# Performance work log

Measured on AMD Instinct MI355X. Metric: run time of the kernel, lower is better.

Reference implementation:

```python
import jax, jax.numpy as jnp
import numpy as np

DIM = 512
WIN = 8
HEADS = 16
HEAD_DIM = DIM // HEADS
N = WIN * WIN
B_ = 1568


def _rel_pos_idx(window_size: int) -> np.ndarray:
    ch = np.arange(window_size)
    cw = np.arange(window_size)
    coords = np.stack(np.meshgrid(ch, cw, indexing='ij'))  # [2, W, W]
    flat = coords.reshape(2, -1)                            # [2, N]
    rel = flat[:, :, None] - flat[:, None, :]               # [2, N, N]
    rel = rel.transpose(1, 2, 0).copy()                     # [N, N, 2]
    rel[:, :, 0] += window_size - 1
    rel[:, :, 1] += window_size - 1
    rel[:, :, 0] *= 2 * window_size - 1
    return rel.sum(-1).astype(np.int32)                     # [N, N]


def setup_inputs() -> dict:
    key = jax.random.key(0)
    kx, kt, kq, kp, kb = jax.random.split(key, 5)
    x = jax.random.normal(kx, (B_, N, DIM), dtype=jnp.float32)
    # learned params
    table = jax.random.normal(kt, ((2 * WIN - 1) ** 2, HEADS), dtype=jnp.float32) * 0.02
    qkv_w = jax.random.normal(kq, (3 * DIM, DIM), dtype=jnp.float32) * (1.0 / np.sqrt(DIM))
    proj_w = jax.random.normal(kp, (DIM, DIM), dtype=jnp.float32) * (1.0 / np.sqrt(DIM))
    proj_b = jax.random.normal(kb, (DIM,), dtype=jnp.float32) * 0.02
    rel_idx = jnp.asarray(_rel_pos_idx(WIN))  # [N, N] int32
    return {"x": x, "qkv_w": qkv_w, "table": table, "proj_w": proj_w,
            "proj_b": proj_b, "rel_idx": rel_idx}


def reference(x, qkv_w, table, proj_w, proj_b, rel_idx):
    Bw, n, c = x.shape
    scale = jnp.sqrt(jnp.float32(HEAD_DIM))
    # qkv: Linear no-bias, torch weight [3C, C] -> x @ W^T
    qkv = (x @ qkv_w.T).reshape(Bw, n, 3, HEADS, HEAD_DIM)
    qkv = jnp.transpose(qkv, (2, 0, 3, 1, 4))  # [3, B, H, N, hd]
    q, k, v = qkv[0], qkv[1], qkv[2]
    attn = jnp.einsum('bhnd,bhmd->bhnm', q, k) / scale  # [B, H, N, N]
    bias = table[rel_idx]                                # [N, N, H]
    attn = attn + jnp.transpose(bias, (2, 0, 1))[None]   # [B, H, N, N]
    attn = jax.nn.softmax(attn, axis=-1)
    out = jnp.einsum('bhnm,bhmd->bhnd', attn, v)         # [B, H, N, hd]
    out = jnp.transpose(out, (0, 2, 1, 3)).reshape(Bw, n, c)
    return out @ proj_w.T + proj_b
```

## Files before the change

kernel.cpp:

```cpp
#include <hip/hip_runtime.h>
#include <stdint.h>

typedef unsigned short ushort_t;
typedef unsigned long long u64_t;
typedef __attribute__((ext_vector_type(4))) float f32x4;
typedef __attribute__((ext_vector_type(8))) short s16x8;

#define S1_ELEMS ((size_t)1568*64*512)

__device__ __forceinline__ ushort_t f2bf(float f) {
  unsigned u = __builtin_bit_cast(unsigned, f);
  u = u + 0x7fffu + ((u >> 16) & 1u);
  return (ushort_t)(u >> 16);
}

__device__ __forceinline__ void gl_lds16(const ushort_t* g, ushort_t* l) {
  typedef __attribute__((address_space(1))) void gvoid;
  typedef __attribute__((address_space(3))) void lvoid;
  __builtin_amdgcn_global_load_lds((gvoid*)(ushort_t*)g, (lvoid*)l, 16, 0, 0);
}

__global__ void k_prep(const float* __restrict__ x, ushort_t* __restrict__ xh,
                       const float* __restrict__ wq, ushort_t* __restrict__ wqh,
                       const float* __restrict__ wp, ushort_t* __restrict__ wph,
                       const float* __restrict__ table, const int* __restrict__ rel_idx,
                       float* __restrict__ bias) {
  int blk = blockIdx.x, tid = threadIdx.x;
  if (blk < 3136) {
    long i0 = (long)blk*256 + tid;
    #pragma unroll
    for (int rep = 0; rep < 8; rep++) {
      long i = i0 + (long)rep*802816;
      float4 v0 = ((const float4*)x)[2*i];
      float4 v1 = ((const float4*)x)[2*i + 1];
      s16x8 pk;
      pk[0] = (short)f2bf(v0.x); pk[1] = (short)f2bf(v0.y);
      pk[2] = (short)f2bf(v0.z); pk[3] = (short)f2bf(v0.w);
      pk[4] = (short)f2bf(v1.x); pk[5] = (short)f2bf(v1.y);
      pk[6] = (short)f2bf(v1.z); pk[7] = (short)f2bf(v1.w);
      *(s16x8*)&xh[i*8] = pk;
    }
  } else if (blk < 3648) {
    const float* src; ushort_t* dst; long i;
    if (blk < 3520) { src = wq; dst = wqh; i = (long)(blk - 3136)*256 + tid; }
    else            { src = wp; dst = wph; i = (long)(blk - 3520)*256 + tid; }
    float4 v0 = ((const float4*)src)[2*i];
    float4 v1 = ((const float4*)src)[2*i + 1];
    s16x8 pk;
    pk[0] = (short)f2bf(v0.x); pk[1] = (short)f2bf(v0.y);
    pk[2] = (short)f2bf(v0.z); pk[3] = (short)f2bf(v0.w);
    pk[4] = (short)f2bf(v1.x); pk[5] = (short)f2bf(v1.y);
    pk[6] = (short)f2bf(v1.z); pk[7] = (short)f2bf(v1.w);
    *(s16x8*)&dst[i*8] = pk;
  } else {
    int i0 = ((blk - 3648)*256 + tid)*4;
    #pragma unroll
    for (int j = 0; j < 4; j++) {
      int i = i0 + j;
      int h = i >> 12, rc = i & 4095;
      bias[i] = table[rel_idx[rc] * 16 + h];
    }
  }
}

struct GemmCtx {
  ushort_t* lds;
  const ushort_t *pA0, *pA1, *pB0, *pB1;
  int w, lane, wm, wn;
};

template<int BUFP, int KH, int RH, int SSEL, int SBUFP, int SU, int VM, bool BAR>
__device__ __forceinline__ void phase(const GemmCtx& C, f32x4 (&acc)[8][4], s16x8 (&bf)[4], int stau) {
  s16x8 af[4];
  #pragma unroll
  for (int t = 0; t < 4; t++)
    af[t] = *(const s16x8*)&C.lds[BUFP*32768 + ((C.wm*8 + RH*4 + t)*2 + KH)*512 + C.lane*8];
  if constexpr (RH == 0) {
    #pragma unroll
    for (int t = 0; t < 4; t++)
      bf[t] = *(const s16x8*)&C.lds[BUFP*32768 + 16384 + ((C.wn*4 + t)*2 + KH)*512 + C.lane*8];
  }
  if constexpr (SSEL == 0) {
    gl_lds16(C.pA0 + stau*64 + SU*32, C.lds + SBUFP*32768 + (4*C.w + SU)*512);
    gl_lds16(C.pA1 + stau*64 + SU*32, C.lds + SBUFP*32768 + (4*C.w + 2 + SU)*512);
  } else if constexpr (SSEL == 1) {
    gl_lds16(C.pB0 + stau*64 + SU*32, C.lds + SBUFP*32768 + 16384 + (4*C.w + SU)*512);
    gl_lds16(C.pB1 + stau*64 + SU*32, C.lds + SBUFP*32768 + 16384 + (4*C.w + 2 + SU)*512);
  }
  if constexpr (VM == 8) asm volatile("s_waitcnt vmcnt(8)" ::: "memory");
  else if constexpr (VM == 4) asm volatile("s_waitcnt vmcnt(4)" ::: "memory");
  else if constexpr (VM == 0) asm volatile("s_waitcnt vmcnt(0)" ::: "memory");
  __builtin_amdgcn_s_setprio(1);
  #pragma unroll
  for (int ta = 0; ta < 4; ta++)
    #pragma unroll
    for (int tb = 0; tb < 4; tb++)
      acc[RH*4 + ta][tb] = __builtin_amdgcn_mfma_f32_16x16x32_bf16(af[ta], bf[tb], acc[RH*4 + ta][tb], 0, 0, 0);
  __builtin_amdgcn_s_setprio(0);
  if constexpr (BAR) __builtin_amdgcn_s_barrier();
}

template<int BUFP, bool S12, bool S34, int VM2, int VM4>
__device__ __forceinline__ void ktile(const GemmCtx& C, f32x4 (&acc)[8][4], int tau) {
  s16x8 bf[4];
  phase<BUFP, 0, 0, S12 ? 0 : -1, BUFP^1, 1, -1,  false>(C, acc, bf, tau + 1);
  phase<BUFP, 0, 1, S12 ? 1 : -1, BUFP^1, 1, VM2, true >(C, acc, bf, tau + 1);
  phase<BUFP, 1, 0, S34 ? 0 : -1, BUFP,   0, -1,  false>(C, acc, bf, tau + 2);
  phase<BUFP, 1, 1, S34 ? 1 : -1, BUFP,   0, VM4, true >(C, acc, bf, tau + 2);
}

__global__ __launch_bounds__(512, 2) void k_gemm_qkv(
    const ushort_t* __restrict__ xh, const ushort_t* __restrict__ wh,
    ushort_t* __restrict__ qh, ushort_t* __restrict__ kh, ushort_t* __restrict__ vt) {
  extern __shared__ __align__(16) ushort_t lds[];
  const int tid = threadIdx.x, w = tid >> 6, lane = tid & 63;
  const int g = lane >> 4, l15 = lane & 15;
  const int wm = w >> 2, wn = w & 3;
  int flat = blockIdx.x;
  int swz = (flat & 7) * 294 + (flat >> 3);
  int bx = swz % 6, by = swz / 6;

  GemmCtx C;
  C.lds = lds;
  C.pA0 = xh + ((size_t)by*256 + (size_t)(2*w)*16 + l15)*512 + g*8;
  C.pA1 = C.pA0 + 16*512;
  C.pB0 = wh + ((size_t)bx*256 + (size_t)(2*w)*16 + l15)*512 + g*8;
  C.pB1 = C.pB0 + 16*512;
  C.w = w; C.lane = lane; C.wm = wm; C.wn = wn;

  f32x4 acc[8][4];
  #pragma unroll
  for (int r = 0; r < 8; r++)
    #pragma unroll
    for (int c = 0; c < 4; c++) acc[r][c] = (f32x4){0.f, 0.f, 0.f, 0.f};

  gl_lds16(C.pA0 +  0, lds + (4*w + 0)*512);
  gl_lds16(C.pA1 +  0, lds + (4*w + 2)*512);
  gl_lds16(C.pB0 +  0, lds + 16384 + (4*w + 0)*512);
  gl_lds16(C.pB1 +  0, lds + 16384 + (4*w + 2)*512);
  gl_lds16(C.pA0 + 32, lds + (4*w + 1)*512);
  gl_lds16(C.pA1 + 32, lds + (4*w + 3)*512);
  gl_lds16(C.pB0 + 32, lds + 16384 + (4*w + 1)*512);
  gl_lds16(C.pB1 + 32, lds + 16384 + (4*w + 3)*512);
  gl_lds16(C.pA0 + 64, lds + 32768 + (4*w + 0)*512);
  gl_lds16(C.pA1 + 64, lds + 32768 + (4*w + 2)*512);
  gl_lds16(C.pB0 + 64, lds + 32768 + 16384 + (4*w + 0)*512);
  gl_lds16(C.pB1 + 64, lds + 32768 + 16384 + (4*w + 2)*512);
  asm volatile("s_waitcnt vmcnt(4)" ::: "memory");
  __builtin_amdgcn_s_barrier();

  for (int kt = 0; kt < 6; kt += 2) {
    ktile<0, true, true, 8, 8>(C, acc, kt);
    ktile<1, true, true, 8, 8>(C, acc, kt + 1);
  }
  ktile<0, true,  false, 8, 4>(C, acc, 6);
  ktile<1, false, false, 0, -1>(C, acc, 7);

  asm volatile("" ::: "memory");
  const int sel = bx >> 1;
  if (sel < 2) {
    #pragma unroll
    for (int ra = 0; ra < 8; ra++)
      #pragma unroll
      for (int tb = 0; tb < 4; tb++)
        #pragma unroll
        for (int j = 0; j < 4; j++) {
          int row = wm*128 + ra*16 + g*4 + j;
          int col = wn*64 + tb*16 + l15;
          int r = (row >> 6)*8 + (col >> 5);
          int n = row & 63, d = col & 31;
          int byte = r*4096 + ((n*64 + d*2) ^ ((n & 12) << 3));
          *(ushort_t*)((char*)lds + byte) = f2bf(acc[ra][tb][j]);
        }
  } else {
    #pragma unroll
    for (int ra = 0; ra < 8; ra++)
      #pragma unroll
      for (int tb = 0; tb < 4; tb++) {
        int row0 = wm*128 + ra*16 + g*4;
        int col = wn*64 + tb*16 + l15;
        int r = (row0 >> 6)*8 + (col >> 5);
        int n0 = row0 & 63, d = col & 31;
        u64_t pk = (u64_t)f2bf(acc[ra][tb][0])
                 | ((u64_t)f2bf(acc[ra][tb][1]) << 16)
                 | ((u64_t)f2bf(acc[ra][tb][2]) << 32)
                 | ((u64_t)f2bf(acc[ra][tb][3]) << 48);
        int byte = r*4096 + ((d*128 + n0*2) ^ ((d & 7) << 4) ^ (((((d >> 3) ^ (n0 >> 3))) & 1) << 6));
        *(u64_t*)((char*)lds + byte) = pk;
      }
  }
  asm volatile("s_waitcnt lgkmcnt(0)" ::: "memory");
  __builtin_amdgcn_s_barrier();
  ushort_t* dst = (sel == 0) ? qh : (sel == 1) ? kh : vt;
  const int hbase = (bx & 1) * 8;
  #pragma unroll
  for (int it = 0; it < 16; it++) {
    int cg = it*512 + tid;
    int r = cg >> 8, inner = cg & 255;
    int byte;
    if (sel < 2) byte = r*4096 + ((inner*16) ^ (((inner >> 2) & 12) << 3));
    else         byte = r*4096 + ((inner*16) ^ (((inner >> 3) & 7) << 4) ^ ((((inner >> 6) ^ inner) & 1) << 6));
    s16x8 v = *(const s16x8*)((const char*)lds + byte);
    int b = by*4 + (r >> 3), h = hbase + (r & 7);
    *(s16x8*)&dst[(size_t)(b*16 + h)*2048 + inner*8] = v;
  }
}

__device__ __forceinline__ void gemm256_loop(
    ushort_t* lds, const ushort_t* pA, const ushort_t* pB,
    int w, int lane, int wm, int wn, f32x4 (&acc)[8][4]) {
  #pragma unroll
  for (int q = 0; q < 2; q++) {
    gl_lds16(pA + q*8192 +  0, lds + ((2*w + q)*2 + 0)*512);
    gl_lds16(pA + q*8192 + 32, lds + ((2*w + q)*2 + 1)*512);
    gl_lds16(pB + q*8192 +  0, lds + 16384 + ((2*w + q)*2 + 0)*512);
    gl_lds16(pB + q*8192 + 32, lds + 16384 + ((2*w + q)*2 + 1)*512);
  }
  asm volatile("s_waitcnt vmcnt(0)" ::: "memory");
  __builtin_amdgcn_s_barrier();

  for (int tau = 0; tau < 8; ++tau) {
    ushort_t* bufR = lds + (tau & 1)*32768;
    ushort_t* bufW = lds + ((tau & 1) ^ 1)*32768;
    if (tau < 7) {
      int ko = (tau + 1)*64;
      #pragma unroll
      for (int q = 0; q < 2; q++) {
        gl_lds16(pA + q*8192 + ko,      bufW + ((2*w + q)*2 + 0)*512);
        gl_lds16(pA + q*8192 + ko + 32, bufW + ((2*w + q)*2 + 1)*512);
        gl_lds16(pB + q*8192 + ko,      bufW + 16384 + ((2*w + q)*2 + 0)*512);
        gl_lds16(pB + q*8192 + ko + 32, bufW + 16384 + ((2*w + q)*2 + 1)*512);
      }
    }
    s16x8 af[4][2], bf[4][2];
    #pragma unroll
    for (int t = 0; t < 4; t++)
      #pragma unroll
      for (int kh = 0; kh < 2; kh++) {
        af[t][kh] = *(const s16x8*)&bufR[((wm*8 + t)*2 + kh)*512 + lane*8];
        bf[t][kh] = *(const s16x8*)&bufR[16384 + ((wn*4 + t)*2 + kh)*512 + lane*8];
      }
    __builtin_amdgcn_s_setprio(1);
    #pragma unroll
    for (int t = 0; t < 4; t++)
      #pragma unroll
      for (int tb = 0; tb < 4; tb++) {
        acc[t][tb] = __builtin_amdgcn_mfma_f32_16x16x32_bf16(af[t][0], bf[tb][0], acc[t][tb], 0, 0, 0);
        acc[t][tb] = __builtin_amdgcn_mfma_f32_16x16x32_bf16(af[t][1], bf[tb][1], acc[t][tb], 0, 0, 0);
      }
    __builtin_amdgcn_s_setprio(0);
    s16x8 ag[4][2];
    #pragma unroll
    for (int t = 0; t < 4; t++)
      #pragma unroll
      for (int kh = 0; kh < 2; kh++)
        ag[t][kh] = *(const s16x8*)&bufR[((wm*8 + 4 + t)*2 + kh)*512 + lane*8];
    __builtin_amdgcn_s_setprio(1);
    #pragma unroll
    for (int t = 0; t < 4; t++)
      #pragma unroll
      for (int tb = 0; tb < 4; tb++) {
        acc[4 + t][tb] = __builtin_amdgcn_mfma_f32_16x16x32_bf16(ag[t][0], bf[tb][0], acc[4 + t][tb], 0, 0, 0);
        acc[4 + t][tb] = __builtin_amdgcn_mfma_f32_16x16x32_bf16(ag[t][1], bf[tb][1], acc[4 + t][tb], 0, 0, 0);
      }
    __builtin_amdgcn_s_setprio(0);
    asm volatile("s_waitcnt vmcnt(0)" ::: "memory");
    __builtin_amdgcn_s_barrier();
  }
}

__global__ __launch_bounds__(512, 2) void k_gemm_proj(
    const ushort_t* __restrict__ ah, const ushort_t* __restrict__ wh,
    const float* __restrict__ pb, float* __restrict__ out) {
  extern __shared__ __align__(16) ushort_t lds[];
  const int tid = threadIdx.x, w = tid >> 6, lane = tid & 63;
  const int g = lane >> 4, l15 = lane & 15;
  const int wm = w >> 2, wn = w & 3;
  int flat = blockIdx.x;
  int swz = (flat & 7) * 98 + (flat >> 3);
  int bx = swz & 1, by = swz >> 1;

  const ushort_t* pA = ah + ((size_t)by*256 + (size_t)(2*w)*16 + l15)*512 + g*8;
  const ushort_t* pB = wh + ((size_t)bx*256 + (size_t)(2*w)*16 + l15)*512 + g*8;

  f32x4 acc[8][4];
  #pragma unroll
  for (int r = 0; r < 8; r++)
    #pragma unroll
    for (int c = 0; c < 4; c++) acc[r][c] = (f32x4){0.f, 0.f, 0.f, 0.f};

  gemm256_loop(lds, pA, pB, w, lane, wm, wn, acc);

  asm volatile("" ::: "memory");
  #pragma unroll
  for (int p = 0; p < 2; p++) {
    if (p) { asm volatile("" ::: "memory"); __builtin_amdgcn_s_barrier(); }
    if (wm == p) {
      #pragma unroll
      for (int ra = 0; ra < 8; ra++)
        #pragma unroll
        for (int tb = 0; tb < 4; tb++)
          #pragma unroll
          for (int j = 0; j < 4; j++) {
            int row = ra*16 + g*4 + j;
            int col = wn*64 + tb*16 + l15;
            int byte = (row*1024 + col*4) ^ ((row & 12) << 2) ^ ((row & 8) << 3);
            *(float*)((char*)lds + byte) = acc[ra][tb][j];
          }
    }
    asm volatile("s_waitcnt lgkmcnt(0)" ::: "memory");
    __builtin_amdgcn_s_barrier();
    #pragma unroll
    for (int it = 0; it < 16; it++) {
      int cg = it*512 + tid;
      int row = cg >> 6, c16 = cg & 63;
      int byte = row*1024 + ((c16*16) ^ ((row & 12) << 2) ^ ((row & 8) << 3));
      f32x4 v = *(const f32x4*)((const char*)lds + byte);
      int ncol = bx*256 + c16*4;
      f32x4 pbv = *(const f32x4*)&pb[ncol];
      v = v + pbv;
      *(f32x4*)&out[(size_t)(by*256 + p*128 + row)*512 + ncol] = v;
    }
  }
}

__global__ __launch_bounds__(256) void k_attn(
    const ushort_t* __restrict__ qh, const ushort_t* __restrict__ kh,
    const ushort_t* __restrict__ vt, const float* __restrict__ bias,
    ushort_t* __restrict__ aoh) {
  __shared__ ushort_t plds[4][64*72];
  __shared__ float blds[64*68];
  const int tid = threadIdx.x, w = tid >> 6, lane = tid & 63;
  const int g = lane >> 4, l15 = lane & 15;
  const int h = blockIdx.x & 15;
  const int b = (blockIdx.x >> 4)*4 + w;
  const size_t base = (size_t)(b*16 + h) * 2048;

  s16x8 qf[4], kf[4];
  #pragma unroll
  for (int t = 0; t < 4; t++) {
    size_t o = base + (size_t)(t*16 + l15)*32 + g*8;
    qf[t] = *(const s16x8*)&qh[o];
    kf[t] = *(const s16x8*)&kh[o];
  }
  s16x8 vf[2][2];
  #pragma unroll
  for (int kt = 0; kt < 2; kt++)
    #pragma unroll
    for (int nt = 0; nt < 2; nt++)
      vf[kt][nt] = *(const s16x8*)&vt[base + (size_t)(nt*16 + l15)*64 + kt*32 + g*8];

  const float* bh_ = bias + ((size_t)h << 12);
  #pragma unroll
  for (int it = 0; it < 4; it++) {
    int idx = it*1024 + tid*4;
    int rr = idx >> 6, cc = idx & 63;
    *(f32x4*)&blds[rr*68 + cc] = *(const f32x4*)&bh_[idx];
  }
  __syncthreads();

  f32x4 s[4][4];
  #pragma unroll
  for (int r = 0; r < 4; r++)
    #pragma unroll
    for (int c = 0; c < 4; c++) s[r][c] = (f32x4){0.f,0.f,0.f,0.f};
  #pragma unroll
  for (int r = 0; r < 4; r++)
    #pragma unroll
    for (int c = 0; c < 4; c++)
      s[r][c] = __builtin_amdgcn_mfma_f32_16x16x32_bf16(qf[r], kf[c], s[r][c], 0, 0, 0);

  const float invs = 0.17677669529663687f;
  #pragma unroll
  for (int r = 0; r < 4; r++)
    #pragma unroll
    for (int c = 0; c < 4; c++)
      #pragma unroll
      for (int j = 0; j < 4; j++) {
        int rr = r*16 + g*4 + j, cc = c*16 + l15;
        s[r][c][j] = s[r][c][j]*invs + blds[rr*68 + cc];
      }

  #pragma unroll
  for (int r = 0; r < 4; r++)
    #pragma unroll
    for (int j = 0; j < 4; j++) {
      float mx = fmaxf(fmaxf(s[r][0][j], s[r][1][j]), fmaxf(s[r][2][j], s[r][3][j]));
      mx = fmaxf(mx, __shfl_xor(mx, 1));
      mx = fmaxf(mx, __shfl_xor(mx, 2));
      mx = fmaxf(mx, __shfl_xor(mx, 4));
      mx = fmaxf(mx, __shfl_xor(mx, 8));
      float p0 = __expf(s[r][0][j]-mx), p1 = __expf(s[r][1][j]-mx);
      float p2 = __expf(s[r][2][j]-mx), p3 = __expf(s[r][3][j]-mx);
      float sum = p0 + p1 + p2 + p3;
      sum += __shfl_xor(sum, 1);
      sum += __shfl_xor(sum, 2);
      sum += __shfl_xor(sum, 4);
      sum += __shfl_xor(sum, 8);
      float rv = 1.0f / sum;
      s[r][0][j] = p0*rv; s[r][1][j] = p1*rv; s[r][2][j] = p2*rv; s[r][3][j] = p3*rv;
    }

  ushort_t* Pm = plds[w];
  #pragma unroll
  for (int r = 0; r < 4; r++)
    #pragma unroll
    for (int c = 0; c < 4; c++)
      #pragma unroll
      for (int j = 0; j < 4; j++) {
        int rr = r*16 + g*4 + j, cc = c*16 + l15;
        Pm[rr*72 + cc] = f2bf(s[r][c][j]);
      }
  s16x8 pf[4][2];
  #pragma unroll
  for (int ta = 0; ta < 4; ta++)
    #pragma unroll
    for (int kt = 0; kt < 2; kt++)
      pf[ta][kt] = *(const s16x8*)&Pm[(ta*16 + l15)*72 + kt*32 + g*8];

  f32x4 o[4][2];
  #pragma unroll
  for (int ta = 0; ta < 4; ta++)
    #pragma unroll
    for (int nt = 0; nt < 2; nt++) o[ta][nt] = (f32x4){0.f,0.f,0.f,0.f};
  #pragma unroll
  for (int ta = 0; ta < 4; ta++)
    #pragma unroll
    for (int nt = 0; nt < 2; nt++)
      #pragma unroll
      for (int kt = 0; kt < 2; kt++)
        o[ta][nt] = __builtin_amdgcn_mfma_f32_16x16x32_bf16(pf[ta][kt], vf[kt][nt], o[ta][nt], 0, 0, 0);

  #pragma unroll
  for (int ta = 0; ta < 4; ta++)
    #pragma unroll
    for (int nt = 0; nt < 2; nt++)
      #pragma unroll
      for (int j = 0; j < 4; j++) {
        int rr = ta*16 + g*4 + j, dd = nt*16 + l15;
        aoh[((size_t)b*64 + rr)*512 + h*32 + dd] = f2bf(o[ta][nt][j]);
      }
}

extern "C" void kernel_launch(void* const* d_in, const int* in_sizes, int n_in,
                              void* d_out, int out_size, void* d_ws, size_t ws_size,
                              hipStream_t stream) {
  const float* x      = (const float*)d_in[0];
  const float* qkv_w  = (const float*)d_in[1];
  const float* table  = (const float*)d_in[2];
  const float* proj_w = (const float*)d_in[3];
  const float* proj_b = (const float*)d_in[4];
  const int*   rel_idx = (const int*)d_in[5];

  const size_t S1 = S1_ELEMS;
  const size_t need = (4*S1 + 786432 + 262144)*sizeof(ushort_t) + 65536*sizeof(float);
  if (ws_size < need) return;

  ushort_t* qh  = (ushort_t*)d_ws;
  ushort_t* kh  = qh + S1;
  ushort_t* vt  = kh + S1;
  ushort_t* xh  = vt + S1;
  ushort_t* wqh = xh + S1;
  ushort_t* wph = wqh + 786432;
  float*    bias = (float*)(wph + 262144);
  ushort_t* aoh = xh;

  hipFuncSetAttribute((const void*)k_gemm_qkv,
                      hipFuncAttributeMaxDynamicSharedMemorySize, 131072);
  hipFuncSetAttribute((const void*)k_gemm_proj,
                      hipFuncAttributeMaxDynamicSharedMemorySize, 131072);

  k_prep<<<3712, 256, 0, stream>>>(x, xh, qkv_w, wqh, proj_w, wph, table, rel_idx, bias);
  k_gemm_qkv<<<2352, 512, 131072, stream>>>(xh, wqh, qh, kh, vt);
  k_attn<<<6272, 256, 0, stream>>>(qh, kh, vt, bias, aoh);
  k_gemm_proj<<<784, 512, 131072, stream>>>(aoh, wph, proj_b, (float*)d_out);
}
```

Measured before the change: 523.4 us.

## Fuse window attention with output projection in one kernel

Replaces the separate attention and projection kernels with one kernel where each 512-thread block handles one window. Each wave computes two heads and writes its attention output to LDS in MFMA fragment layout. The block then runs the 64x512x512 projection GEMM directly from LDS, streaming projection-weight slices through a double buffer. This removes the global round trip of the bf16 attention output and one launch. In exchange, every block re-reads the full projection weight from L2. The 128KB LDS footprint limits occupancy, and the bias table is now read from global memory instead of being staged in LDS.

```diff
diff --git a/kernel.cpp b/kernel.cpp
--- a/kernel.cpp
+++ b/kernel.cpp
@@ -206,239 +206,185 @@
   }
 }
 
-__device__ __forceinline__ void gemm256_loop(
-    ushort_t* lds, const ushort_t* pA, const ushort_t* pB,
-    int w, int lane, int wm, int wn, f32x4 (&acc)[8][4]) {
-  #pragma unroll
-  for (int q = 0; q < 2; q++) {
-    gl_lds16(pA + q*8192 +  0, lds + ((2*w + q)*2 + 0)*512);
-    gl_lds16(pA + q*8192 + 32, lds + ((2*w + q)*2 + 1)*512);
-    gl_lds16(pB + q*8192 +  0, lds + 16384 + ((2*w + q)*2 + 0)*512);
-    gl_lds16(pB + q*8192 + 32, lds + 16384 + ((2*w + q)*2 + 1)*512);
-  }
-  asm volatile("s_waitcnt vmcnt(0)" ::: "memory");
-  __builtin_amdgcn_s_barrier();
-
-  for (int tau = 0; tau < 8; ++tau) {
-    ushort_t* bufR = lds + (tau & 1)*32768;
-    ushort_t* bufW = lds + ((tau & 1) ^ 1)*32768;
-    if (tau < 7) {
-      int ko = (tau + 1)*64;
-      #pragma unroll
-      for (int q = 0; q < 2; q++) {
-        gl_lds16(pA + q*8192 + ko,      bufW + ((2*w + q)*2 + 0)*512);
-        gl_lds16(pA + q*8192 + ko + 32, bufW + ((2*w + q)*2 + 1)*512);
-        gl_lds16(pB + q*8192 + ko,      bufW + 16384 + ((2*w + q)*2 + 0)*512);
-        gl_lds16(pB + q*8192 + ko + 32, bufW + 16384 + ((2*w + q)*2 + 1)*512);
-      }
-    }
-    s16x8 af[4][2], bf[4][2];
-    #pragma unroll
-    for (int t = 0; t < 4; t++)
-      #pragma unroll
-      for (int kh = 0; kh < 2; kh++) {
-        af[t][kh] = *(const s16x8*)&bufR[((wm*8 + t)*2 + kh)*512 + lane*8];
-        bf[t][kh] = *(const s16x8*)&bufR[16384 + ((wn*4 + t)*2 + kh)*512 + lane*8];
-      }
-    __builtin_amdgcn_s_setprio(1);
-    #pragma unroll
-    for (int t = 0; t < 4; t++)
-      #pragma unroll
-      for (int tb = 0; tb < 4; tb++) {
-        acc[t][tb] = __builtin_amdgcn_mfma_f32_16x16x32_bf16(af[t][0], bf[tb][0], acc[t][tb], 0, 0, 0);
-        acc[t][tb] = __builtin_amdgcn_mfma_f32_16x16x32_bf16(af[t][1], bf[tb][1], acc[t][tb], 0, 0, 0);
-      }
-    __builtin_amdgcn_s_setprio(0);
-    s16x8 ag[4][2];
-    #pragma unroll
-    for (int t = 0; t < 4; t++)
-      #pragma unroll
-      for (int kh = 0; kh < 2; kh++)
-        ag[t][kh] = *(const s16x8*)&bufR[((wm*8 + 4 + t)*2 + kh)*512 + lane*8];
-    __builtin_amdgcn_s_setprio(1);
-    #pragma unroll
-    for (int t = 0; t < 4; t++)
-      #pragma unroll
-      for (int tb = 0; tb < 4; tb++) {
-        acc[4 + t][tb] = __builtin_amdgcn_mfma_f32_16x16x32_bf16(ag[t][0], bf[tb][0], acc[4 + t][tb], 0, 0, 0);
-        acc[4 + t][tb] = __builtin_amdgcn_mfma_f32_16x16x32_bf16(ag[t][1], bf[tb][1], acc[4 + t][tb], 0, 0, 0);
-      }
-    __builtin_amdgcn_s_setprio(0);
-    asm volatile("s_waitcnt vmcnt(0)" ::: "memory");
-    __builtin_amdgcn_s_barrier();
-  }
-}
-
-__global__ __launch_bounds__(512, 2) void k_gemm_proj(
-    const ushort_t* __restrict__ ah, const ushort_t* __restrict__ wh,
-    const float* __restrict__ pb, float* __restrict__ out) {
+__global__ __launch_bounds__(512) void k_attn_proj(
+    const ushort_t* __restrict__ qh, const ushort_t* __restrict__ kh,
+    const ushort_t* __restrict__ vt, const float* __restrict__ bias,
+    const ushort_t* __restrict__ wph, const float* __restrict__ pb,
+    float* __restrict__ out) {
   extern __shared__ __align__(16) ushort_t lds[];
+  ushort_t* aoL = lds;
+  ushort_t* pP  = lds + 32768;
   const int tid = threadIdx.x, w = tid >> 6, lane = tid & 63;
   const int g = lane >> 4, l15 = lane & 15;
-  const int wm = w >> 2, wn = w & 3;
-  int flat = blockIdx.x;
-  int swz = (flat & 7) * 98 + (flat >> 3);
-  int bx = swz & 1, by = swz >> 1;
-
-  const ushort_t* pA = ah + ((size_t)by*256 + (size_t)(2*w)*16 + l15)*512 + g*8;
-  const ushort_t* pB = wh + ((size_t)bx*256 + (size_t)(2*w)*16 + l15)*512 + g*8;
-
-  f32x4 acc[8][4];
-  #pragma unroll
-  for (int r = 0; r < 8; r++)
+  const int b = blockIdx.x;
+
+  #pragma unroll
+  for (int hw = 0; hw < 2; hw++) {
+    const int h = w*2 + hw;
+    const size_t base = ((size_t)b*16 + h) * 2048;
+
+    s16x8 qf[4], kf[4];
+    #pragma unroll
+    for (int t = 0; t < 4; t++) {
+      size_t o = base + (size_t)(t*16 + l15)*32 + g*8;
+      qf[t] = *(const s16x8*)&qh[o];
+      kf[t] = *(const s16x8*)&kh[o];
+    }
+    s16x8 vf[2][2];
+    #pragma unroll
+    for (int kt = 0; kt < 2; kt++)
+      #pragma unroll
+      for (int nt = 0; nt < 2; nt++)
+        vf[kt][nt] = *(const s16x8*)&vt[base + (size_t)(nt*16 + l15)*64 + kt*32 + g*8];
+
+    f32x4 s[4][4];
+    #pragma unroll
+    for (int r = 0; r < 4; r++)
+      #pragma unroll
+      for (int c = 0; c < 4; c++) s[r][c] = (f32x4){0.f,0.f,0.f,0.f};
+    #pragma unroll
+    for (int r = 0; r < 4; r++)
+      #pragma unroll
+      for (int c = 0; c < 4; c++)
+        s[r][c] = __builtin_amdgcn_mfma_f32_16x16x32_bf16(qf[r], kf[c], s[r][c], 0, 0, 0);
+
+    const float invs = 0.17677669529663687f;
+    const float* bh_ = bias + ((size_t)h << 12);
+    #pragma unroll
+    for (int r = 0; r < 4; r++)
+      #pragma unroll
+      for (int c = 0; c < 4; c++)
+        #pragma unroll
+        for (int j = 0; j < 4; j++) {
+          int rr = r*16 + g*4 + j, cc = c*16 + l15;
+          s[r][c][j] = s[r][c][j]*invs + bh_[rr*64 + cc];
+        }
+
+    #pragma unroll
+    for (int r = 0; r < 4; r++)
+      #pragma unroll
+      for (int j = 0; j < 4; j++) {
+        float mx = fmaxf(fmaxf(s[r][0][j], s[r][1][j]), fmaxf(s[r][2][j], s[r][3][j]));
+        mx = fmaxf(mx, __shfl_xor(mx, 1));
+        mx = fmaxf(mx, __shfl_xor(mx, 2));
+        mx = fmaxf(mx, __shfl_xor(mx, 4));
+        mx = fmaxf(mx, __shfl_xor(mx, 8));
+        float p0 = __expf(s[r][0][j]-mx), p1 = __expf(s[r][1][j]-mx);
+        float p2 = __expf(s[r][2][j]-mx), p3 = __expf(s[r][3][j]-mx);
+        float sum = p0 + p1 + p2 + p3;
+        sum += __shfl_xor(sum, 1);
+        sum += __shfl_xor(sum, 2);
+        sum += __shfl_xor(sum, 4);
+        sum += __shfl_xor(sum, 8);
+        float rv = 1.0f / sum;
+        s[r][0][j] = p0*rv; s[r][1][j] = p1*rv; s[r][2][j] = p2*rv; s[r][3][j] = p3*rv;
+      }
+
+    ushort_t* Pw = pP + w*4096;
+    asm volatile("s_waitcnt lgkmcnt(0)" ::: "memory");
+    __builtin_amdgcn_sched_barrier(0);
+    #pragma unroll
+    for (int r = 0; r < 4; r++)
+      #pragma unroll
+      for (int c = 0; c < 4; c++)
+        #pragma unroll
+        for (int j = 0; j < 4; j++) {
+          int idx = ((c >> 1)*4 + r)*512 + ((((c & 1)*2) + (l15 >> 3))*16 + g*4 + j)*8 + (l15 & 7);
+          Pw[idx] = f2bf(s[r][c][j]);
+        }
+    asm volatile("s_waitcnt lgkmcnt(0)" ::: "memory");
+    __builtin_amdgcn_sched_barrier(0);
+
+    s16x8 pf[4][2];
+    #pragma unroll
+    for (int ta = 0; ta < 4; ta++)
+      #pragma unroll
+      for (int kt = 0; kt < 2; kt++)
+        pf[ta][kt] = *(const s16x8*)&Pw[(kt*4 + ta)*512 + lane*8];
+
+    f32x4 o[4][2];
+    #pragma unroll
+    for (int ta = 0; ta < 4; ta++)
+      #pragma unroll
+      for (int nt = 0; nt < 2; nt++) o[ta][nt] = (f32x4){0.f,0.f,0.f,0.f};
+    #pragma unroll
+    for (int ta = 0; ta < 4; ta++)
+      #pragma unroll
+      for (int nt = 0; nt < 2; nt++)
+        #pragma unroll
+        for (int kt = 0; kt < 2; kt++)
+          o[ta][nt] = __builtin_amdgcn_mfma_f32_16x16x32_bf16(pf[ta][kt], vf[kt][nt], o[ta][nt], 0, 0, 0);
+
+    #pragma unroll
+    for (int ta = 0; ta < 4; ta++)
+      #pragma unroll
+      for (int nt = 0; nt < 2; nt++)
+        #pragma unroll
+        for (int j = 0; j < 4; j++) {
+          int idx = (h*4 + ta)*512 + ((nt*2 + (l15 >> 3))*16 + g*4 + j)*8 + (l15 & 7);
+          aoL[idx] = f2bf(o[ta][nt][j]);
+        }
+  }
+
+  __syncthreads();
+
+  f32x4 acc[4][4];
+  #pragma unroll
+  for (int r = 0; r < 4; r++)
     #pragma unroll
     for (int c = 0; c < 4; c++) acc[r][c] = (f32x4){0.f, 0.f, 0.f, 0.f};
 
-  gemm256_loop(lds, pA, pB, w, lane, wm, wn, acc);
-
-  asm volatile("" ::: "memory");
-  #pragma unroll
-  for (int p = 0; p < 2; p++) {
-    if (p) { asm volatile("" ::: "memory"); __builtin_amdgcn_s_barrier(); }
-    if (wm == p) {
-      #pragma unroll
-      for (int ra = 0; ra < 8; ra++)
-        #pragma unroll
-        for (int tb = 0; tb < 4; tb++)
-          #pragma unroll
-          for (int j = 0; j < 4; j++) {
-            int row = ra*16 + g*4 + j;
-            int col = wn*64 + tb*16 + l15;
-            int byte = (row*1024 + col*4) ^ ((row & 12) << 2) ^ ((row & 8) << 3);
-            *(float*)((char*)lds + byte) = acc[ra][tb][j];
-          }
+  ushort_t* buf0 = pP;
+  ushort_t* buf1 = pP + 16384;
+  const ushort_t* bsrc[4];
+  #pragma unroll
+  for (int q = 0; q < 4; q++)
+    bsrc[q] = wph + (size_t)((4*w + q)*16 + l15)*512 + g*8;
+
+  #pragma unroll
+  for (int q = 0; q < 4; q++)
+    gl_lds16(bsrc[q], buf0 + (4*w + q)*512);
+
+  for (int t = 0; t < 16; ++t) {
+    ushort_t* bufR = (t & 1) ? buf1 : buf0;
+    ushort_t* bufW = (t & 1) ? buf0 : buf1;
+    if (t < 15) {
+      #pragma unroll
+      for (int q = 0; q < 4; q++)
+        gl_lds16(bsrc[q] + (t + 1)*32, bufW + (4*w + q)*512);
+      asm volatile("s_waitcnt vmcnt(4)" ::: "memory");
+    } else {
+      asm volatile("s_waitcnt vmcnt(0)" ::: "memory");
     }
-    asm volatile("s_waitcnt lgkmcnt(0)" ::: "memory");
-    __builtin_amdgcn_s_barrier();
-    #pragma unroll
-    for (int it = 0; it < 16; it++) {
-      int cg = it*512 + tid;
-      int row = cg >> 6, c16 = cg & 63;
-      int byte = row*1024 + ((c16*16) ^ ((row & 12) << 2) ^ ((row & 8) << 3));
-      f32x4 v = *(const f32x4*)((const char*)lds + byte);
-      int ncol = bx*256 + c16*4;
-      f32x4 pbv = *(const f32x4*)&pb[ncol];
-      v = v + pbv;
-      *(f32x4*)&out[(size_t)(by*256 + p*128 + row)*512 + ncol] = v;
-    }
-  }
-}
-
-__global__ __launch_bounds__(256) void k_attn(
-    const ushort_t* __restrict__ qh, const ushort_t* __restrict__ kh,
-    const ushort_t* __restrict__ vt, const float* __restrict__ bias,
-    ushort_t* __restrict__ aoh) {
-  __shared__ ushort_t plds[4][64*72];
-  __shared__ float blds[64*68];
-  const int tid = threadIdx.x, w = tid >> 6, lane = tid & 63;
-  const int g = lane >> 4, l15 = lane & 15;
-  const int h = blockIdx.x & 15;
-  const int b = (blockIdx.x >> 4)*4 + w;
-  const size_t base = (size_t)(b*16 + h) * 2048;
-
-  s16x8 qf[4], kf[4];
-  #pragma unroll
-  for (int t = 0; t < 4; t++) {
-    size_t o = base + (size_t)(t*16 + l15)*32 + g*8;
-    qf[t] = *(const s16x8*)&qh[o];
-    kf[t] = *(const s16x8*)&kh[o];
-  }
-  s16x8 vf[2][2];
-  #pragma unroll
-  for (int kt = 0; kt < 2; kt++)
-    #pragma unroll
-    for (int nt = 0; nt < 2; nt++)
-      vf[kt][nt] = *(const s16x8*)&vt[base + (size_t)(nt*16 + l15)*64 + kt*32 + g*8];
-
-  const float* bh_ = bias + ((size_t)h << 12);
-  #pragma unroll
-  for (int it = 0; it < 4; it++) {
-    int idx = it*1024 + tid*4;
-    int rr = idx >> 6, cc = idx & 63;
-    *(f32x4*)&blds[rr*68 + cc] = *(const f32x4*)&bh_[idx];
-  }
-  __syncthreads();
-
-  f32x4 s[4][4];
-  #pragma unroll
-  for (int r = 0; r < 4; r++)
-    #pragma unroll
-    for (int c = 0; c < 4; c++) s[r][c] = (f32x4){0.f,0.f,0.f,0.f};
-  #pragma unroll
-  for (int r = 0; r < 4; r++)
-    #pragma unroll
-    for (int c = 0; c < 4; c++)
-      s[r][c] = __builtin_amdgcn_mfma_f32_16x16x32_bf16(qf[r], kf[c], s[r][c], 0, 0, 0);
-
-  const float invs = 0.17677669529663687f;
-  #pragma unroll
-  for (int r = 0; r < 4; r++)
-    #pragma unroll
-    for (int c = 0; c < 4; c++)
+    __builtin_amdgcn_sched_barrier(0);
+    s16x8 af[4], bf[4];
+    #pragma unroll
+    for (int ta = 0; ta < 4; ta++)
+      af[ta] = *(const s16x8*)&aoL[(t*4 + ta)*512 + lane*8];
+    #pragma unroll
+    for (int tb = 0; tb < 4; tb++)
+      bf[tb] = *(const s16x8*)&bufR[(w*4 + tb)*512 + lane*8];
+    __builtin_amdgcn_s_setprio(1);
+    #pragma unroll
+    for (int ta = 0; ta < 4; ta++)
+      #pragma unroll
+      for (int tb = 0; tb < 4; tb++)
+        acc[ta][tb] = __builtin_amdgcn_mfma_f32_16x16x32_bf16(af[ta], bf[tb], acc[ta][tb], 0, 0, 0);
+    __builtin_amdgcn_s_setprio(0);
+  }
+
+  float pbv[4];
+  #pragma unroll
+  for (int tb = 0; tb < 4; tb++) pbv[tb] = pb[w*64 + tb*16 + l15];
+  #pragma unroll
+  for (int ta = 0; ta < 4; ta++)
+    #pragma unroll
+    for (int tb = 0; tb < 4; tb++)
       #pragma unroll
       for (int j = 0; j < 4; j++) {
-        int rr = r*16 + g*4 + j, cc = c*16 + l15;
-        s[r][c][j] = s[r][c][j]*invs + blds[rr*68 + cc];
-      }
-
-  #pragma unroll
-  for (int r = 0; r < 4; r++)
-    #pragma unroll
-    for (int j = 0; j < 4; j++) {
-      float mx = fmaxf(fmaxf(s[r][0][j], s[r][1][j]), fmaxf(s[r][2][j], s[r][3][j]));
-      mx = fmaxf(mx, __shfl_xor(mx, 1));
-      mx = fmaxf(mx, __shfl_xor(mx, 2));
-      mx = fmaxf(mx, __shfl_xor(mx, 4));
-      mx = fmaxf(mx, __shfl_xor(mx, 8));
-      float p0 = __expf(s[r][0][j]-mx), p1 = __expf(s[r][1][j]-mx);
-      float p2 = __expf(s[r][2][j]-mx), p3 = __expf(s[r][3][j]-mx);
-      float sum = p0 + p1 + p2 + p3;
-      sum += __shfl_xor(sum, 1);
-      sum += __shfl_xor(sum, 2);
-      sum += __shfl_xor(sum, 4);
-      sum += __shfl_xor(sum, 8);
-      float rv = 1.0f / sum;
-      s[r][0][j] = p0*rv; s[r][1][j] = p1*rv; s[r][2][j] = p2*rv; s[r][3][j] = p3*rv;
-    }
-
-  ushort_t* Pm = plds[w];
-  #pragma unroll
-  for (int r = 0; r < 4; r++)
-    #pragma unroll
-    for (int c = 0; c < 4; c++)
-      #pragma unroll
-      for (int j = 0; j < 4; j++) {
-        int rr = r*16 + g*4 + j, cc = c*16 + l15;
-        Pm[rr*72 + cc] = f2bf(s[r][c][j]);
-      }
-  s16x8 pf[4][2];
-  #pragma unroll
-  for (int ta = 0; ta < 4; ta++)
-    #pragma unroll
-    for (int kt = 0; kt < 2; kt++)
-      pf[ta][kt] = *(const s16x8*)&Pm[(ta*16 + l15)*72 + kt*32 + g*8];
-
-  f32x4 o[4][2];
-  #pragma unroll
-  for (int ta = 0; ta < 4; ta++)
-    #pragma unroll
-    for (int nt = 0; nt < 2; nt++) o[ta][nt] = (f32x4){0.f,0.f,0.f,0.f};
-  #pragma unroll
-  for (int ta = 0; ta < 4; ta++)
-    #pragma unroll
-    for (int nt = 0; nt < 2; nt++)
-      #pragma unroll
-      for (int kt = 0; kt < 2; kt++)
-        o[ta][nt] = __builtin_amdgcn_mfma_f32_16x16x32_bf16(pf[ta][kt], vf[kt][nt], o[ta][nt], 0, 0, 0);
-
-  #pragma unroll
-  for (int ta = 0; ta < 4; ta++)
-    #pragma unroll
-    for (int nt = 0; nt < 2; nt++)
-      #pragma unroll
-      for (int j = 0; j < 4; j++) {
-        int rr = ta*16 + g*4 + j, dd = nt*16 + l15;
-        aoh[((size_t)b*64 + rr)*512 + h*32 + dd] = f2bf(o[ta][nt][j]);
+        int row = ta*16 + g*4 + j;
+        int col = w*64 + tb*16 + l15;
+        out[((size_t)b*64 + row)*512 + col] = acc[ta][tb][j] + pbv[tb];
       }
 }
 
@@ -463,15 +409,13 @@
   ushort_t* wqh = xh + S1;
   ushort_t* wph = wqh + 786432;
   float*    bias = (float*)(wph + 262144);
-  ushort_t* aoh = xh;
 
   hipFuncSetAttribute((const void*)k_gemm_qkv,
                       hipFuncAttributeMaxDynamicSharedMemorySize, 131072);
-  hipFuncSetAttribute((const void*)k_gemm_proj,
+  hipFuncSetAttribute((const void*)k_attn_proj,
                       hipFuncAttributeMaxDynamicSharedMemorySize, 131072);
 
   k_prep<<<3712, 256, 0, stream>>>(x, xh, qkv_w, wqh, proj_w, wph, table, rel_idx, bias);
   k_gemm_qkv<<<2352, 512, 131072, stream>>>(xh, wqh, qh, kh, vt);
-  k_attn<<<6272, 256, 0, stream>>>(qh, kh, vt, bias, aoh);
-  k_gemm_proj<<<784, 512, 131072, stream>>>(aoh, wph, proj_b, (float*)d_out);
-}
+  k_attn_proj<<<1568, 512, 131072, stream>>>(qh, kh, vt, bias, wph, proj_b, (float*)d_out);
+}
```

After: 562.0 us, median of 2. 1.07x slower.

## Reuse pipelined QKV GEMM loop for projection and pack P in MFMA fragment layout

Applied to the files above, without the earlier changes.

The projection GEMM drops its simple double-buffered loop and calls the same phased, software-pipelined k-loop as the QKV GEMM, through a shared helper. The goal is to overlap global-to-LDS loads with MFMA work better in the output projection. In the attention kernel, the softmax probabilities are now written to LDS directly in MFMA operand-fragment order. Each lane then reads its fragment as one contiguous 16-byte load, which removes the padded strided layout. Explicit lgkmcnt waits and scheduling barriers are added around the P store, which may serialize some work.

```diff
diff --git a/kernel.cpp b/kernel.cpp
--- a/kernel.cpp
+++ b/kernel.cpp
@@ -109,31 +109,9 @@
   phase<BUFP, 1, 1, S34 ? 1 : -1, BUFP,   0, VM4, true >(C, acc, bf, tau + 2);
 }
 
-__global__ __launch_bounds__(512, 2) void k_gemm_qkv(
-    const ushort_t* __restrict__ xh, const ushort_t* __restrict__ wh,
-    ushort_t* __restrict__ qh, ushort_t* __restrict__ kh, ushort_t* __restrict__ vt) {
-  extern __shared__ __align__(16) ushort_t lds[];
-  const int tid = threadIdx.x, w = tid >> 6, lane = tid & 63;
-  const int g = lane >> 4, l15 = lane & 15;
-  const int wm = w >> 2, wn = w & 3;
-  int flat = blockIdx.x;
-  int swz = (flat & 7) * 294 + (flat >> 3);
-  int bx = swz % 6, by = swz / 6;
-
-  GemmCtx C;
-  C.lds = lds;
-  C.pA0 = xh + ((size_t)by*256 + (size_t)(2*w)*16 + l15)*512 + g*8;
-  C.pA1 = C.pA0 + 16*512;
-  C.pB0 = wh + ((size_t)bx*256 + (size_t)(2*w)*16 + l15)*512 + g*8;
-  C.pB1 = C.pB0 + 16*512;
-  C.w = w; C.lane = lane; C.wm = wm; C.wn = wn;
-
-  f32x4 acc[8][4];
-  #pragma unroll
-  for (int r = 0; r < 8; r++)
-    #pragma unroll
-    for (int c = 0; c < 4; c++) acc[r][c] = (f32x4){0.f, 0.f, 0.f, 0.f};
-
+__device__ __forceinline__ void run_gemm_loop(const GemmCtx& C, f32x4 (&acc)[8][4]) {
+  ushort_t* lds = C.lds;
+  const int w = C.w;
   gl_lds16(C.pA0 +  0, lds + (4*w + 0)*512);
   gl_lds16(C.pA1 +  0, lds + (4*w + 2)*512);
   gl_lds16(C.pB0 +  0, lds + 16384 + (4*w + 0)*512);
@@ -155,6 +133,34 @@
   }
   ktile<0, true,  false, 8, 4>(C, acc, 6);
   ktile<1, false, false, 0, -1>(C, acc, 7);
+}
+
+__global__ __launch_bounds__(512, 2) void k_gemm_qkv(
+    const ushort_t* __restrict__ xh, const ushort_t* __restrict__ wh,
+    ushort_t* __restrict__ qh, ushort_t* __restrict__ kh, ushort_t* __restrict__ vt) {
+  extern __shared__ __align__(16) ushort_t lds[];
+  const int tid = threadIdx.x, w = tid >> 6, lane = tid & 63;
+  const int g = lane >> 4, l15 = lane & 15;
+  const int wm = w >> 2, wn = w & 3;
+  int flat = blockIdx.x;
+  int swz = (flat & 7) * 294 + (flat >> 3);
+  int bx = swz % 6, by = swz / 6;
+
+  GemmCtx C;
+  C.lds = lds;
+  C.pA0 = xh + ((size_t)by*256 + (size_t)(2*w)*16 + l15)*512 + g*8;
+  C.pA1 = C.pA0 + 16*512;
+  C.pB0 = wh + ((size_t)bx*256 + (size_t)(2*w)*16 + l15)*512 + g*8;
+  C.pB1 = C.pB0 + 16*512;
+  C.w = w; C.lane = lane; C.wm = wm; C.wn = wn;
+
+  f32x4 acc[8][4];
+  #pragma unroll
+  for (int r = 0; r < 8; r++)
+    #pragma unroll
+    for (int c = 0; c < 4; c++) acc[r][c] = (f32x4){0.f, 0.f, 0.f, 0.f};
+
+  run_gemm_loop(C, acc);
 
   asm volatile("" ::: "memory");
   const int sel = bx >> 1;
@@ -206,69 +212,6 @@
   }
 }
 
-__device__ __forceinline__ void gemm256_loop(
-    ushort_t* lds, const ushort_t* pA, const ushort_t* pB,
-    int w, int lane, int wm, int wn, f32x4 (&acc)[8][4]) {
-  #pragma unroll
-  for (int q = 0; q < 2; q++) {
-    gl_lds16(pA + q*8192 +  0, lds + ((2*w + q)*2 + 0)*512);
-    gl_lds16(pA + q*8192 + 32, lds + ((2*w + q)*2 + 1)*512);
-    gl_lds16(pB + q*8192 +  0, lds + 16384 + ((2*w + q)*2 + 0)*512);
-    gl_lds16(pB + q*8192 + 32, lds + 16384 + ((2*w + q)*2 + 1)*512);
-  }
-  asm volatile("s_waitcnt vmcnt(0)" ::: "memory");
-  __builtin_amdgcn_s_barrier();
-
-  for (int tau = 0; tau < 8; ++tau) {
-    ushort_t* bufR = lds + (tau & 1)*32768;
-    ushort_t* bufW = lds + ((tau & 1) ^ 1)*32768;
-    if (tau < 7) {
-      int ko = (tau + 1)*64;
-      #pragma unroll
-      for (int q = 0; q < 2; q++) {
-        gl_lds16(pA + q*8192 + ko,      bufW + ((2*w + q)*2 + 0)*512);
-        gl_lds16(pA + q*8192 + ko + 32, bufW + ((2*w + q)*2 + 1)*512);
-        gl_lds16(pB + q*8192 + ko,      bufW + 16384 + ((2*w + q)*2 + 0)*512);
-        gl_lds16(pB + q*8192 + ko + 32, bufW + 16384 + ((2*w + q)*2 + 1)*512);
-      }
-    }
-    s16x8 af[4][2], bf[4][2];
-    #pragma unroll
-    for (int t = 0; t < 4; t++)
-      #pragma unroll
-      for (int kh = 0; kh < 2; kh++) {
-        af[t][kh] = *(const s16x8*)&bufR[((wm*8 + t)*2 + kh)*512 + lane*8];
-        bf[t][kh] = *(const s16x8*)&bufR[16384 + ((wn*4 + t)*2 + kh)*512 + lane*8];
-      }
-    __builtin_amdgcn_s_setprio(1);
-    #pragma unroll
-    for (int t = 0; t < 4; t++)
-      #pragma unroll
-      for (int tb = 0; tb < 4; tb++) {
-        acc[t][tb] = __builtin_amdgcn_mfma_f32_16x16x32_bf16(af[t][0], bf[tb][0], acc[t][tb], 0, 0, 0);
-        acc[t][tb] = __builtin_amdgcn_mfma_f32_16x16x32_bf16(af[t][1], bf[tb][1], acc[t][tb], 0, 0, 0);
-      }
-    __builtin_amdgcn_s_setprio(0);
-    s16x8 ag[4][2];
-    #pragma unroll
-    for (int t = 0; t < 4; t++)
-      #pragma unroll
-      for (int kh = 0; kh < 2; kh++)
-        ag[t][kh] = *(const s16x8*)&bufR[((wm*8 + 4 + t)*2 + kh)*512 + lane*8];
-    __builtin_amdgcn_s_setprio(1);
-    #pragma unroll
-    for (int t = 0; t < 4; t++)
-      #pragma unroll
-      for (int tb = 0; tb < 4; tb++) {
-        acc[4 + t][tb] = __builtin_amdgcn_mfma_f32_16x16x32_bf16(ag[t][0], bf[tb][0], acc[4 + t][tb], 0, 0, 0);
-        acc[4 + t][tb] = __builtin_amdgcn_mfma_f32_16x16x32_bf16(ag[t][1], bf[tb][1], acc[4 + t][tb], 0, 0, 0);
-      }
-    __builtin_amdgcn_s_setprio(0);
-    asm volatile("s_waitcnt vmcnt(0)" ::: "memory");
-    __builtin_amdgcn_s_barrier();
-  }
-}
-
 __global__ __launch_bounds__(512, 2) void k_gemm_proj(
     const ushort_t* __restrict__ ah, const ushort_t* __restrict__ wh,
     const float* __restrict__ pb, float* __restrict__ out) {
@@ -280,8 +223,13 @@
   int swz = (flat & 7) * 98 + (flat >> 3);
   int bx = swz & 1, by = swz >> 1;
 
-  const ushort_t* pA = ah + ((size_t)by*256 + (size_t)(2*w)*16 + l15)*512 + g*8;
-  const ushort_t* pB = wh + ((size_t)bx*256 + (size_t)(2*w)*16 + l15)*512 + g*8;
+  GemmCtx C;
+  C.lds = lds;
+  C.pA0 = ah + ((size_t)by*256 + (size_t)(2*w)*16 + l15)*512 + g*8;
+  C.pA1 = C.pA0 + 16*512;
+  C.pB0 = wh + ((size_t)bx*256 + (size_t)(2*w)*16 + l15)*512 + g*8;
+  C.pB1 = C.pB0 + 16*512;
+  C.w = w; C.lane = lane; C.wm = wm; C.wn = wn;
 
   f32x4 acc[8][4];
   #pragma unroll
@@ -289,7 +237,7 @@
     #pragma unroll
     for (int c = 0; c < 4; c++) acc[r][c] = (f32x4){0.f, 0.f, 0.f, 0.f};
 
-  gemm256_loop(lds, pA, pB, w, lane, wm, wn, acc);
+  run_gemm_loop(C, acc);
 
   asm volatile("" ::: "memory");
   #pragma unroll
@@ -328,7 +276,7 @@
     const ushort_t* __restrict__ qh, const ushort_t* __restrict__ kh,
     const ushort_t* __restrict__ vt, const float* __restrict__ bias,
     ushort_t* __restrict__ aoh) {
-  __shared__ ushort_t plds[4][64*72];
+  __shared__ ushort_t plds[4][4096];
   __shared__ float blds[64*68];
   const int tid = threadIdx.x, w = tid >> 6, lane = tid & 63;
   const int g = lane >> 4, l15 = lane & 15;
@@ -401,22 +349,27 @@
       s[r][0][j] = p0*rv; s[r][1][j] = p1*rv; s[r][2][j] = p2*rv; s[r][3][j] = p3*rv;
     }
 
-  ushort_t* Pm = plds[w];
+  ushort_t* Pw = plds[w];
+  asm volatile("s_waitcnt lgkmcnt(0)" ::: "memory");
+  __builtin_amdgcn_sched_barrier(0);
   #pragma unroll
   for (int r = 0; r < 4; r++)
     #pragma unroll
     for (int c = 0; c < 4; c++)
       #pragma unroll
       for (int j = 0; j < 4; j++) {
-        int rr = r*16 + g*4 + j, cc = c*16 + l15;
-        Pm[rr*72 + cc] = f2bf(s[r][c][j]);
+        int idx = ((c >> 1)*4 + r)*512 + ((((c & 1)*2) + (l15 >> 3))*16 + g*4 + j)*8 + (l15 & 7);
+        Pw[idx] = f2bf(s[r][c][j]);
       }
+  asm volatile("s_waitcnt lgkmcnt(0)" ::: "memory");
+  __builtin_amdgcn_sched_barrier(0);
+
   s16x8 pf[4][2];
   #pragma unroll
   for (int ta = 0; ta < 4; ta++)
     #pragma unroll
     for (int kt = 0; kt < 2; kt++)
-      pf[ta][kt] = *(const s16x8*)&Pm[(ta*16 + l15)*72 + kt*32 + g*8];
+      pf[ta][kt] = *(const s16x8*)&Pw[(kt*4 + ta)*512 + lane*8];
 
   f32x4 o[4][2];
   #pragma unroll
```

Measured after the change: 508.0 us. 1.03x faster.
